# Kernel optimization log

Hardware: AMD Instinct MI355X
Metric: run time of the kernel (lower is better)

## Reference

```python
import math
import jax, jax.numpy as jnp
import numpy as np

S = 2048
D_MOD = 1024
D_K = 64
D_V = 64
H = 16
MASKED = True


def setup_inputs() -> dict:
    key = jax.random.key(0)
    ks = jax.random.split(key, 11)
    sc_in = 1.0 / math.sqrt(D_MOD)
    sc_o = 1.0 / math.sqrt(H * D_V)
    return {
        "Q_input": jax.random.normal(ks[0], (S, D_MOD), jnp.float32),
        "K_input": jax.random.normal(ks[1], (S, D_MOD), jnp.float32),
        "V_input": jax.random.normal(ks[2], (S, D_MOD), jnp.float32),
        # stacked per-head Linear params (torch Linear: y = x @ W.T + b)
        "WQw": jax.random.uniform(ks[3], (H, D_K, D_MOD), jnp.float32, -sc_in, sc_in),
        "WQb": jax.random.uniform(ks[4], (H, D_K), jnp.float32, -sc_in, sc_in),
        "WKw": jax.random.uniform(ks[5], (H, D_K, D_MOD), jnp.float32, -sc_in, sc_in),
        "WKb": jax.random.uniform(ks[6], (H, D_K), jnp.float32, -sc_in, sc_in),
        "WVw": jax.random.uniform(ks[7], (H, D_V, D_MOD), jnp.float32, -sc_in, sc_in),
        "WVb": jax.random.uniform(ks[8], (H, D_V), jnp.float32, -sc_in, sc_in),
        "WOw": jax.random.uniform(ks[9], (D_MOD, H * D_V), jnp.float32, -sc_o, sc_o),
        "WOb": jax.random.uniform(ks[10], (D_MOD,), jnp.float32, -sc_o, sc_o),
    }


def reference(Q_input, K_input, V_input, WQw, WQb, WKw, WKb, WVw, WVb, WOw, WOb):
    # per-head projections, batched over heads: [H, S, d]
    q = jnp.einsum("sd,hkd->hsk", Q_input, WQw) + WQb[:, None, :]
    k = jnp.einsum("sd,hkd->hsk", K_input, WKw) + WKb[:, None, :]
    v = jnp.einsum("sd,hvd->hsv", V_input, WVw) + WVb[:, None, :]
    # raw scores [H, S, T]
    qk = jnp.einsum("hsk,htk->hst", q, k)
    if MASKED:
        qk = jnp.tril(qk)  # torch.tril: zero (not -inf) upper triangle
    # torch log_softmax(dim=0) on each [S, T] matrix -> axis 1 of [H, S, T]
    scores = jax.nn.log_softmax(qk / math.sqrt(D_K), axis=1)
    attn = jnp.einsum("hst,htv->hsv", scores, v)  # [H, S, d_v]
    # torch.cat(head_attns, dim=1) -> [S, H*d_v], head-major feature order
    Z = jnp.transpose(attn, (1, 0, 2)).reshape(S, H * D_V)
    return Z @ WOw.T + WOb
```

## Files before the change

kernel.cpp:

```cpp
#include <hip/hip_runtime.h>
#include <math.h>
#include <stdint.h>

#define S 2048
#define DMOD 1024
#define H 16

typedef unsigned short ushort_t;
typedef short bf16x8 __attribute__((ext_vector_type(8)));
typedef float f32x4 __attribute__((ext_vector_type(4)));

#define SW(r) ((((r) & 7)) ^ ((((r) >> 3) & 3) << 1))

__device__ __forceinline__ ushort_t f2b(float f) {
    union { float f; unsigned u; } x; x.f = f;
    return (ushort_t)((x.u + 0x7FFFu + ((x.u >> 16) & 1u)) >> 16);
}
__device__ __forceinline__ ushort_t f2b_fast(float f) {
    union { float f; unsigned u; } x; x.f = f;
    return (ushort_t)((x.u + 0x8000u) >> 16);
}
__device__ __forceinline__ float b2f(ushort_t b) {
    union { unsigned u; float f; } x; x.u = ((unsigned)b) << 16;
    return x.f;
}
__device__ __forceinline__ void gld16(const ushort_t* g, ushort_t* l) {
    __builtin_amdgcn_global_load_lds(
        (const __attribute__((address_space(1))) unsigned int*)g,
        (__attribute__((address_space(3))) unsigned int*)l, 16, 0, 0);
}

__global__ __launch_bounds__(256) void prep_all(
    const float* q, const float* k, const float* v,
    const float* wq, const float* wk, const float* wv, const float* wo,
    ushort_t* qo, ushort_t* ko, ushort_t* vo,
    ushort_t* wqo, ushort_t* wko, ushort_t* wvo, ushort_t* woo,
    float* __restrict__ attn_raw, float* __restrict__ out,
    float* __restrict__ sumexp, float* __restrict__ corr)
{
    const int seg = blockIdx.y;
    const int bx = blockIdx.x;
    if (seg >= 10) {
        const float4 z4 = {0.f, 0.f, 0.f, 0.f};
        if (seg < 12) {
            *(float4*)(attn_raw + (((size_t)(seg - 10) * 1024 + bx) * 256 + threadIdx.x) * 4) = z4;
        } else if (seg < 14) {
            *(float4*)(out + (((size_t)(seg - 12) * 1024 + bx) * 256 + threadIdx.x) * 4) = z4;
        } else if (bx < 32) {
            int e = (bx * 256 + threadIdx.x) * 4;
            float4 vv = {(float)(e & 2047), (float)((e + 1) & 2047),
                         (float)((e + 2) & 2047), (float)((e + 3) & 2047)};
            *(float4*)(sumexp + e) = vv;
        } else if (bx == 32) {
            *(float4*)(corr + threadIdx.x * 4) = z4;
        }
        return;
    }
    const float* src; ushort_t* dst; size_t off = 0;
    const size_t M1 = (size_t)1 << 20;
    if (seg < 2)       { src = q;  dst = qo;  off = (size_t)seg * M1; }
    else if (seg < 4)  { src = k;  dst = ko;  off = (size_t)(seg - 2) * M1; }
    else if (seg < 6)  { src = v;  dst = vo;  off = (size_t)(seg - 4) * M1; }
    else if (seg == 6) { src = wq; dst = wqo; }
    else if (seg == 7) { src = wk; dst = wko; }
    else if (seg == 8) { src = wv; dst = wvo; }
    else               { src = wo; dst = woo; }
    size_t i = off + ((size_t)bx * 256 + threadIdx.x) * 4;
    float4 f = *(const float4*)(src + i);
    union { uint2 u2; ushort_t us[4]; } o;
    o.us[0] = f2b(f.x); o.us[1] = f2b(f.y); o.us[2] = f2b(f.z); o.us[3] = f2b(f.w);
    *(uint2*)(dst + i) = o.u2;
}

__global__ __launch_bounds__(256) void gemm_qkv(
    const ushort_t* __restrict__ A0, const ushort_t* __restrict__ A1,
    const ushort_t* __restrict__ A2, const ushort_t* __restrict__ Wqkv,
    const float* __restrict__ b0, const float* __restrict__ b1,
    const float* __restrict__ b2,
    ushort_t* __restrict__ qbb, ushort_t* __restrict__ kbb,
    ushort_t* __restrict__ vt)
{
    __shared__ ushort_t As[128 * 64];
    __shared__ ushort_t Bs[64 * 64];
    const int tid = threadIdx.x;
    const int lane = tid & 63, wid = tid >> 6;
    const int quad = lane >> 4, l15 = lane & 15;
    const int wr = wid >> 1, wc = wid & 1;
    const int m0 = blockIdx.y * 128;
    const int n0 = blockIdx.x * 64;
    const int seg = n0 >> 10;
    const int nloc = n0 & 1023;
    const ushort_t* A = seg == 0 ? A0 : (seg == 1 ? A1 : A2);
    const float* bias = seg == 0 ? b0 : (seg == 1 ? b1 : b2);

    const f32x4 fz = {0.f, 0.f, 0.f, 0.f};
    f32x4 acc[4][2];
#pragma unroll
    for (int i = 0; i < 4; ++i) { acc[i][0] = fz; acc[i][1] = fz; }

    for (int k0 = 0; k0 < DMOD; k0 += 64) {
        __syncthreads();
#pragma unroll
        for (int i = 0; i < 4; ++i) {
            int c = i * 256 + tid, row = c >> 3, kcl = c & 7;
            gld16(A + (size_t)(m0 + row) * DMOD + k0 + (kcl ^ SW(row)) * 8, &As[c * 8]);
        }
#pragma unroll
        for (int i = 0; i < 2; ++i) {
            int c = i * 256 + tid, row = c >> 3, kcl = c & 7;
            gld16(Wqkv + (size_t)(n0 + row) * DMOD + k0 + (kcl ^ SW(row)) * 8, &Bs[c * 8]);
        }
        __syncthreads();
#pragma unroll
        for (int kc = 0; kc < 2; ++kc) {
            bf16x8 af[4], bfr[2];
#pragma unroll
            for (int mi = 0; mi < 4; ++mi) {
                int row = wr * 64 + mi * 16 + l15;
                af[mi] = *(const bf16x8*)&As[row * 64 + ((kc * 4 + quad) ^ SW(row)) * 8];
            }
#pragma unroll
            for (int ni = 0; ni < 2; ++ni) {
                int row = wc * 32 + ni * 16 + l15;
                bfr[ni] = *(const bf16x8*)&Bs[row * 64 + ((kc * 4 + quad) ^ SW(row)) * 8];
            }
#pragma unroll
            for (int mi = 0; mi < 4; ++mi)
#pragma unroll
                for (int ni = 0; ni < 2; ++ni)
                    acc[mi][ni] = __builtin_amdgcn_mfma_f32_16x16x32_bf16(
                        af[mi], bfr[ni], acc[mi][ni], 0, 0, 0);
        }
    }

    if (seg < 2) {
        ushort_t* C = seg == 0 ? qbb : kbb;
#pragma unroll
        for (int mi = 0; mi < 4; ++mi)
#pragma unroll
            for (int ni = 0; ni < 2; ++ni) {
                int gn = nloc + wc * 32 + ni * 16 + l15;
                float bv = bias[gn];
#pragma unroll
                for (int r = 0; r < 4; ++r) {
                    int gm = m0 + wr * 64 + mi * 16 + quad * 4 + r;
                    C[(size_t)gm * DMOD + gn] = f2b(acc[mi][ni][r] + bv);
                }
            }
    } else {
#pragma unroll
        for (int mi = 0; mi < 4; ++mi)
#pragma unroll
            for (int ni = 0; ni < 2; ++ni) {
                int gn = nloc + wc * 32 + ni * 16 + l15;
                float bv = bias[gn];
                int gmb = m0 + wr * 64 + mi * 16 + quad * 4;
                union { uint2 u2; ushort_t us[4]; } o;
#pragma unroll
                for (int r = 0; r < 4; ++r) o.us[r] = f2b(acc[mi][ni][r] + bv);
                *(uint2*)&vt[(size_t)gn * S + gmb] = o.u2;
            }
    }
}

__global__ __launch_bounds__(512, 4) void attn_mfma(
    const ushort_t* __restrict__ qb, const ushort_t* __restrict__ kb,
    const ushort_t* __restrict__ vt, float* __restrict__ attn_raw,
    float* __restrict__ sumexp)
{
    __shared__ ushort_t QPs[128 * 64];
    __shared__ ushort_t Ks[2][4096];
    __shared__ ushort_t Vs[2][4096];
    __shared__ float    sacc[1024];

    const int slot = blockIdx.x;
    const int h = slot >> 4, u = slot & 15;
    const int rnd = blockIdx.y;
    int si, tbeg, tend;
    if (rnd == 0) { si = 15 - u; tbeg = 0; tend = si + 1; }
    else {
        si = u;
        const int b0 = u + 1, Bc = (u + 2) >> 1;
        if (rnd == 1) { tbeg = b0; tend = b0 + Bc; }
        else          { tbeg = b0 + Bc; tend = 2 * u + 2; }
    }
    if (tbeg >= tend) return;
    const int s0 = si * 128;

    const int tid = threadIdx.x;
    const int lane = tid & 63, w = tid >> 6;
    const int quad = lane >> 4, l15 = lane & 15;
    const int sband = s0 + w * 16;
    const int nv = (tend - tbeg) * 64;

    const ushort_t* qh = qb + h * 64;
    const ushort_t* kh = kb + h * 64;
    const ushort_t* vh = vt + (size_t)(h * 64) * S;

#pragma unroll
    for (int i = 0; i < 2; ++i) {
        int c = i * 512 + tid, row = c >> 3, kcl = c & 7;
        gld16(qh + (size_t)(s0 + row) * DMOD + (kcl ^ SW(row)) * 8, &QPs[c * 8]);
    }
    {
        int t0 = tbeg * 64;
        int row = tid >> 3, kcl = tid & 7;
        gld16(kh + (size_t)(t0 + row) * DMOD + (kcl ^ SW(row)) * 8, &Ks[0][tid * 8]);
        gld16(vh + (size_t)row * S + t0 + (kcl ^ SW(row)) * 8, &Vs[0][tid * 8]);
    }
    for (int i = tid; i < nv; i += 512) sacc[i] = 0.f;
    __syncthreads();

    bf16x8 aq[2];
    {
        int rq = w * 16 + l15;
#pragma unroll
        for (int kc = 0; kc < 2; ++kc)
            aq[kc] = *(const bf16x8*)&QPs[rq * 64 + ((kc * 4 + quad) ^ SW(rq)) * 8];
    }

    const f32x4 fz = {0.f, 0.f, 0.f, 0.f};
    f32x4 oacc[4];
#pragma unroll
    for (int ni = 0; ni < 4; ++ni) oacc[ni] = fz;
    bool any_live = false;

    for (int it = tbeg; it < tend; ++it) {
        const int p = (it - tbeg) & 1;
        const int t0 = it * 64;
        if (it + 1 < tend) {
            int t1 = t0 + 64;
            int row = tid >> 3, kcl = tid & 7;
            gld16(kh + (size_t)(t1 + row) * DMOD + (kcl ^ SW(row)) * 8, &Ks[1 - p][tid * 8]);
            gld16(vh + (size_t)row * S + t1 + (kcl ^ SW(row)) * 8, &Vs[1 - p][tid * 8]);
        }

        if (t0 < sband + 16) {
            any_live = true;
            f32x4 xf[4];
#pragma unroll
            for (int ti = 0; ti < 4; ++ti) xf[ti] = fz;
#pragma unroll
            for (int kc = 0; kc < 2; ++kc) {
#pragma unroll
                for (int ti = 0; ti < 4; ++ti) {
                    int rk = ti * 16 + l15;
                    bf16x8 bk = *(const bf16x8*)&Ks[p][rk * 64 + ((kc * 4 + quad) ^ SW(rk)) * 8];
                    xf[ti] = __builtin_amdgcn_mfma_f32_16x16x32_bf16(aq[kc], bk, xf[ti], 0, 0, 0);
                }
            }

            const bool clean = (t0 + 63 <= sband);
            const int s_q = sband + quad * 4;
#pragma unroll
            for (int ti = 0; ti < 4; ++ti) {
                int t_g = t0 + ti * 16 + l15;
                float es = 0.f;
                if (clean) {
#pragma unroll
                    for (int r = 0; r < 4; ++r) {
                        float xv = xf[ti][r] * 0.125f;
                        es += __expf(xv);
                        xf[ti][r] = xv;
                    }
                } else {
#pragma unroll
                    for (int r = 0; r < 4; ++r) {
                        float xv = xf[ti][r] * 0.125f;
                        bool live = (s_q + r >= t_g);
                        xv = live ? xv : 0.f;
                        es += live ? __expf(xv) : 0.f;
                        xf[ti][r] = xv;
                    }
                }
                es += __shfl_xor(es, 16, 64);
                es += __shfl_xor(es, 32, 64);
                if (quad == 0) atomicAdd(&sacc[(it - tbeg) * 64 + ti * 16 + l15], es);
#pragma unroll
                for (int r = 0; r < 4; ++r) {
                    int sl = w * 16 + quad * 4 + r;
                    int tc = ti * 16 + l15;
                    QPs[sl * 64 + ((tc >> 3) ^ SW(sl)) * 8 + (tc & 7)] = f2b_fast(xf[ti][r]);
                }
            }

#pragma unroll
            for (int kc = 0; kc < 2; ++kc) {
                int rp = w * 16 + l15;
                bf16x8 ap = *(const bf16x8*)&QPs[rp * 64 + ((kc * 4 + quad) ^ SW(rp)) * 8];
#pragma unroll
                for (int ni = 0; ni < 4; ++ni) {
                    int rv = ni * 16 + l15;
                    bf16x8 bv = *(const bf16x8*)&Vs[p][rv * 64 + ((kc * 4 + quad) ^ SW(rv)) * 8];
                    oacc[ni] = __builtin_amdgcn_mfma_f32_16x16x32_bf16(ap, bv, oacc[ni], 0, 0, 0);
                }
            }
        }
        __syncthreads();
    }

    for (int i = tid; i < nv; i += 512)
        atomicAdd(&sumexp[h * S + tbeg * 64 + i], sacc[i]);
    if (any_live) {
#pragma unroll
        for (int ni = 0; ni < 4; ++ni)
#pragma unroll
            for (int r = 0; r < 4; ++r) {
                int s_g = s0 + w * 16 + quad * 4 + r;
                atomicAdd(&attn_raw[(size_t)s_g * DMOD + h * 64 + ni * 16 + l15],
                          oacc[ni][r]);
            }
    }
}

__global__ __launch_bounds__(256) void corr_kernel(
    const float* __restrict__ sumexp, const ushort_t* __restrict__ vt,
    float* __restrict__ corr)
{
    __shared__ float ls[S];
    const int h = blockIdx.x >> 2;
    const int r0 = blockIdx.x * 16;
    const int tid = threadIdx.x;
    for (int t = tid; t < S; t += 256)
        ls[t] = __logf(sumexp[h * S + t]);
    __syncthreads();
    const int w = tid >> 6, lane = tid & 63;
#pragma unroll
    for (int rr = 0; rr < 4; ++rr) {
        int r = r0 + w * 4 + rr;
        float acc = 0.f;
#pragma unroll
        for (int i = 0; i < 4; ++i) {
            int t = i * 512 + lane * 8;
            bf16x8 vv = *(const bf16x8*)&vt[(size_t)r * S + t];
#pragma unroll
            for (int j = 0; j < 8; ++j)
                acc += ls[t + j] * b2f((ushort_t)vv[j]);
        }
#pragma unroll
        for (int d = 1; d < 64; d <<= 1) acc += __shfl_xor(acc, d, 64);
        if (lane == 0) corr[r] = acc;
    }
}

__global__ __launch_bounds__(256) void convert_Z(
    const float* __restrict__ attn_raw, const float* __restrict__ corr,
    ushort_t* __restrict__ Zb)
{
    size_t i = ((size_t)blockIdx.x * 256 + threadIdx.x) * 4;
    float4 f = *(const float4*)(attn_raw + i);
    int c = (int)(i & (DMOD - 1));
    union { uint2 u2; ushort_t us[4]; } o;
    o.us[0] = f2b(f.x - corr[c]);
    o.us[1] = f2b(f.y - corr[c + 1]);
    o.us[2] = f2b(f.z - corr[c + 2]);
    o.us[3] = f2b(f.w - corr[c + 3]);
    *(uint2*)(Zb + i) = o.u2;
}

__global__ __launch_bounds__(256) void gemm_out(
    const ushort_t* __restrict__ A, const ushort_t* __restrict__ W,
    const float* __restrict__ bias, float* __restrict__ C)
{
    __shared__ ushort_t As[128 * 64];
    __shared__ ushort_t Bs[64 * 64];
    const int tid = threadIdx.x;
    const int lane = tid & 63, wid = tid >> 6;
    const int quad = lane >> 4, l15 = lane & 15;
    const int wr = wid >> 1, wc = wid & 1;
    const int m0 = blockIdx.y * 128, n0 = blockIdx.x * 64;

    const f32x4 fz = {0.f, 0.f, 0.f, 0.f};
    f32x4 acc[4][2];
#pragma unroll
    for (int i = 0; i < 4; ++i) { acc[i][0] = fz; acc[i][1] = fz; }

    for (int k0 = 0; k0 < DMOD; k0 += 64) {
        __syncthreads();
#pragma unroll
        for (int i = 0; i < 4; ++i) {
            int c = i * 256 + tid, row = c >> 3, kcl = c & 7;
            gld16(A + (size_t)(m0 + row) * DMOD + k0 + (kcl ^ SW(row)) * 8, &As[c * 8]);
        }
#pragma unroll
        for (int i = 0; i < 2; ++i) {
            int c = i * 256 + tid, row = c >> 3, kcl = c & 7;
            gld16(W + (size_t)(n0 + row) * DMOD + k0 + (kcl ^ SW(row)) * 8, &Bs[c * 8]);
        }
        __syncthreads();
#pragma unroll
        for (int kc = 0; kc < 2; ++kc) {
            bf16x8 af[4], bfr[2];
#pragma unroll
            for (int mi = 0; mi < 4; ++mi) {
                int row = wr * 64 + mi * 16 + l15;
                af[mi] = *(const bf16x8*)&As[row * 64 + ((kc * 4 + quad) ^ SW(row)) * 8];
            }
#pragma unroll
            for (int ni = 0; ni < 2; ++ni) {
                int row = wc * 32 + ni * 16 + l15;
                bfr[ni] = *(const bf16x8*)&Bs[row * 64 + ((kc * 4 + quad) ^ SW(row)) * 8];
            }
#pragma unroll
            for (int mi = 0; mi < 4; ++mi)
#pragma unroll
                for (int ni = 0; ni < 2; ++ni)
                    acc[mi][ni] = __builtin_amdgcn_mfma_f32_16x16x32_bf16(
                        af[mi], bfr[ni], acc[mi][ni], 0, 0, 0);
        }
    }
#pragma unroll
    for (int mi = 0; mi < 4; ++mi)
#pragma unroll
        for (int ni = 0; ni < 2; ++ni) {
            int gn = n0 + wc * 32 + ni * 16 + l15;
            float bv = bias[gn];
#pragma unroll
            for (int r = 0; r < 4; ++r) {
                int gm = m0 + wr * 64 + mi * 16 + quad * 4 + r;
                C[(size_t)gm * DMOD + gn] = acc[mi][ni][r] + bv;
            }
        }
}

extern "C" void kernel_launch(void* const* d_in, const int* in_sizes, int n_in,
                              void* d_out, int out_size, void* d_ws, size_t ws_size,
                              hipStream_t stream) {
    const float* Qin = (const float*)d_in[0];
    const float* Kin = (const float*)d_in[1];
    const float* Vin = (const float*)d_in[2];
    const float* WQw = (const float*)d_in[3];
    const float* WQb = (const float*)d_in[4];
    const float* WKw = (const float*)d_in[5];
    const float* WKb = (const float*)d_in[6];
    const float* WVw = (const float*)d_in[7];
    const float* WVb = (const float*)d_in[8];
    const float* WOw = (const float*)d_in[9];
    const float* WOb = (const float*)d_in[10];

    float* ws = (float*)d_ws;
    const size_t M1 = (size_t)1 << 20;
    ushort_t* qbb  = (ushort_t*)(ws);
    ushort_t* kbb  = (ushort_t*)(ws + M1);
    ushort_t* vt   = (ushort_t*)(ws + 2 * M1);
    ushort_t* wqkv = (ushort_t*)(ws + 3 * M1);
    ushort_t* wob  = (ushort_t*)(ws + 4 * M1 + M1 / 2);
    ushort_t* Qbin = (ushort_t*)(ws + 5 * M1);
    ushort_t* Kbin = (ushort_t*)(ws + 6 * M1);
    ushort_t* Vbin = (ushort_t*)(ws + 7 * M1);
    float* sumexp   = ws + 8 * M1;
    float* corr     = ws + 8 * M1 + H * S;
    float* attn_raw = ws + 9 * M1;
    ushort_t* Zb    = (ushort_t*)(ws + 5 * M1);

    prep_all<<<dim3(1024, 15), 256, 0, stream>>>(
        Qin, Kin, Vin, WQw, WKw, WVw, WOw,
        Qbin, Kbin, Vbin,
        wqkv, wqkv + (size_t)1024 * 1024, wqkv + (size_t)2 * 1024 * 1024, wob,
        attn_raw, (float*)d_out, sumexp, corr);

    gemm_qkv<<<dim3(48, 16), 256, 0, stream>>>(
        Qbin, Kbin, Vbin, wqkv, WQb, WKb, WVb, qbb, kbb, vt);

    attn_mfma<<<dim3(256, 3), 512, 0, stream>>>(qbb, kbb, vt, attn_raw, sumexp);

    corr_kernel<<<64, 256, 0, stream>>>(sumexp, vt, corr);
    convert_Z<<<2048, 256, 0, stream>>>(attn_raw, corr, Zb);

    gemm_out<<<dim3(16, 16), 256, 0, stream>>>(Zb, wob, WOb, (float*)d_out);
}
```

Before: 183.9 us.

## Load Q/K/V MFMA operands directly from global memory instead of LDS staging

Removes the LDS double-buffered K/V tiles and the Q staging buffer in the attention kernel; each wave now loads its MFMA operands straight from global memory (relying on L1/L2 caching) and drops the per-iteration block barrier. The goal is to cut LDS traffic, cp-async staging and __syncthreads stalls and to free shared memory for higher occupancy. In exchange there is no explicit prefetch, and the 8 waves redundantly fetch the same K/V tile from cache, which adds global/L2 load pressure and exposes latency. The P tile stays in LDS, written and read per wave, with no barrier between iterations.

```diff
diff --git a/kernel.cpp b/kernel.cpp
--- a/kernel.cpp
+++ b/kernel.cpp
@@ -168,9 +168,7 @@
     const ushort_t* __restrict__ vt, float* __restrict__ attn_raw,
     float* __restrict__ sumexp)
 {
-    __shared__ ushort_t QPs[128 * 64];
-    __shared__ ushort_t Ks[2][4096];
-    __shared__ ushort_t Vs[2][4096];
+    __shared__ ushort_t Ps[128 * 64];
     __shared__ float    sacc[1024];
 
     const int slot = blockIdx.x;
@@ -193,31 +191,18 @@
     const int sband = s0 + w * 16;
     const int nv = (tend - tbeg) * 64;
 
-    const ushort_t* qh = qb + h * 64;
-    const ushort_t* kh = kb + h * 64;
-    const ushort_t* vh = vt + (size_t)(h * 64) * S;
-
-#pragma unroll
-    for (int i = 0; i < 2; ++i) {
-        int c = i * 512 + tid, row = c >> 3, kcl = c & 7;
-        gld16(qh + (size_t)(s0 + row) * DMOD + (kcl ^ SW(row)) * 8, &QPs[c * 8]);
-    }
-    {
-        int t0 = tbeg * 64;
-        int row = tid >> 3, kcl = tid & 7;
-        gld16(kh + (size_t)(t0 + row) * DMOD + (kcl ^ SW(row)) * 8, &Ks[0][tid * 8]);
-        gld16(vh + (size_t)row * S + t0 + (kcl ^ SW(row)) * 8, &Vs[0][tid * 8]);
-    }
     for (int i = tid; i < nv; i += 512) sacc[i] = 0.f;
-    __syncthreads();
 
     bf16x8 aq[2];
     {
-        int rq = w * 16 + l15;
-#pragma unroll
-        for (int kc = 0; kc < 2; ++kc)
-            aq[kc] = *(const bf16x8*)&QPs[rq * 64 + ((kc * 4 + quad) ^ SW(rq)) * 8];
-    }
+        const ushort_t* qrow = qb + (size_t)(sband + l15) * DMOD + h * 64 + quad * 8;
+        aq[0] = *(const bf16x8*)(qrow);
+        aq[1] = *(const bf16x8*)(qrow + 32);
+    }
+    __syncthreads();
+
+    const ushort_t* kbase = kb + h * 64;
+    const ushort_t* vbase = vt + (size_t)(h * 64) * S;
 
     const f32x4 fz = {0.f, 0.f, 0.f, 0.f};
     f32x4 oacc[4];
@@ -226,78 +211,70 @@
     bool any_live = false;
 
     for (int it = tbeg; it < tend; ++it) {
-        const int p = (it - tbeg) & 1;
         const int t0 = it * 64;
-        if (it + 1 < tend) {
-            int t1 = t0 + 64;
-            int row = tid >> 3, kcl = tid & 7;
-            gld16(kh + (size_t)(t1 + row) * DMOD + (kcl ^ SW(row)) * 8, &Ks[1 - p][tid * 8]);
-            gld16(vh + (size_t)row * S + t1 + (kcl ^ SW(row)) * 8, &Vs[1 - p][tid * 8]);
-        }
-
-        if (t0 < sband + 16) {
-            any_live = true;
-            f32x4 xf[4];
-#pragma unroll
-            for (int ti = 0; ti < 4; ++ti) xf[ti] = fz;
-#pragma unroll
-            for (int kc = 0; kc < 2; ++kc) {
-#pragma unroll
-                for (int ti = 0; ti < 4; ++ti) {
-                    int rk = ti * 16 + l15;
-                    bf16x8 bk = *(const bf16x8*)&Ks[p][rk * 64 + ((kc * 4 + quad) ^ SW(rk)) * 8];
-                    xf[ti] = __builtin_amdgcn_mfma_f32_16x16x32_bf16(aq[kc], bk, xf[ti], 0, 0, 0);
+        if (t0 >= sband + 16) continue;
+        any_live = true;
+
+        f32x4 xf[4];
+#pragma unroll
+        for (int ti = 0; ti < 4; ++ti) xf[ti] = fz;
+#pragma unroll
+        for (int kc = 0; kc < 2; ++kc) {
+#pragma unroll
+            for (int ti = 0; ti < 4; ++ti) {
+                bf16x8 bk = *(const bf16x8*)(kbase +
+                    (size_t)(t0 + ti * 16 + l15) * DMOD + kc * 32 + quad * 8);
+                xf[ti] = __builtin_amdgcn_mfma_f32_16x16x32_bf16(aq[kc], bk, xf[ti], 0, 0, 0);
+            }
+        }
+
+        const bool clean = (t0 + 63 <= sband);
+        const int s_q = sband + quad * 4;
+#pragma unroll
+        for (int ti = 0; ti < 4; ++ti) {
+            int t_g = t0 + ti * 16 + l15;
+            float es = 0.f;
+            if (clean) {
+#pragma unroll
+                for (int r = 0; r < 4; ++r) {
+                    float xv = xf[ti][r] * 0.125f;
+                    es += __expf(xv);
+                    xf[ti][r] = xv;
                 }
-            }
-
-            const bool clean = (t0 + 63 <= sband);
-            const int s_q = sband + quad * 4;
-#pragma unroll
-            for (int ti = 0; ti < 4; ++ti) {
-                int t_g = t0 + ti * 16 + l15;
-                float es = 0.f;
-                if (clean) {
-#pragma unroll
-                    for (int r = 0; r < 4; ++r) {
-                        float xv = xf[ti][r] * 0.125f;
-                        es += __expf(xv);
-                        xf[ti][r] = xv;
-                    }
-                } else {
-#pragma unroll
-                    for (int r = 0; r < 4; ++r) {
-                        float xv = xf[ti][r] * 0.125f;
-                        bool live = (s_q + r >= t_g);
-                        xv = live ? xv : 0.f;
-                        es += live ? __expf(xv) : 0.f;
-                        xf[ti][r] = xv;
-                    }
+            } else {
+#pragma unroll
+                for (int r = 0; r < 4; ++r) {
+                    float xv = xf[ti][r] * 0.125f;
+                    bool live = (s_q + r >= t_g);
+                    xv = live ? xv : 0.f;
+                    es += live ? __expf(xv) : 0.f;
+                    xf[ti][r] = xv;
                 }
-                es += __shfl_xor(es, 16, 64);
-                es += __shfl_xor(es, 32, 64);
-                if (quad == 0) atomicAdd(&sacc[(it - tbeg) * 64 + ti * 16 + l15], es);
-#pragma unroll
-                for (int r = 0; r < 4; ++r) {
-                    int sl = w * 16 + quad * 4 + r;
-                    int tc = ti * 16 + l15;
-                    QPs[sl * 64 + ((tc >> 3) ^ SW(sl)) * 8 + (tc & 7)] = f2b_fast(xf[ti][r]);
-                }
-            }
-
-#pragma unroll
-            for (int kc = 0; kc < 2; ++kc) {
-                int rp = w * 16 + l15;
-                bf16x8 ap = *(const bf16x8*)&QPs[rp * 64 + ((kc * 4 + quad) ^ SW(rp)) * 8];
-#pragma unroll
-                for (int ni = 0; ni < 4; ++ni) {
-                    int rv = ni * 16 + l15;
-                    bf16x8 bv = *(const bf16x8*)&Vs[p][rv * 64 + ((kc * 4 + quad) ^ SW(rv)) * 8];
-                    oacc[ni] = __builtin_amdgcn_mfma_f32_16x16x32_bf16(ap, bv, oacc[ni], 0, 0, 0);
-                }
-            }
-        }
-        __syncthreads();
-    }
+            }
+            es += __shfl_xor(es, 16, 64);
+            es += __shfl_xor(es, 32, 64);
+            if (quad == 0) atomicAdd(&sacc[(it - tbeg) * 64 + ti * 16 + l15], es);
+#pragma unroll
+            for (int r = 0; r < 4; ++r) {
+                int sl = w * 16 + quad * 4 + r;
+                int tc = ti * 16 + l15;
+                Ps[sl * 64 + ((tc >> 3) ^ SW(sl)) * 8 + (tc & 7)] = f2b_fast(xf[ti][r]);
+            }
+        }
+
+#pragma unroll
+        for (int kc = 0; kc < 2; ++kc) {
+            int rp = w * 16 + l15;
+            bf16x8 ap = *(const bf16x8*)&Ps[rp * 64 + ((kc * 4 + quad) ^ SW(rp)) * 8];
+#pragma unroll
+            for (int ni = 0; ni < 4; ++ni) {
+                bf16x8 bv = *(const bf16x8*)(vbase +
+                    (size_t)(ni * 16 + l15) * S + t0 + kc * 32 + quad * 8);
+                oacc[ni] = __builtin_amdgcn_mfma_f32_16x16x32_bf16(ap, bv, oacc[ni], 0, 0, 0);
+            }
+        }
+    }
+    __syncthreads();
 
     for (int i = tid; i < nv; i += 512)
         atomicAdd(&sumexp[h * S + tbeg * 64 + i], sacc[i]);
```

New measurement: 223.4 us. +21.4%, slower.
